# Performance work log

Measured on AMD Instinct MI355X. Metric: run time of the kernel, lower is better.

## Reference

```python
import jax, jax.numpy as jnp
import numpy as np

NUM_CAPSULES = 16
IN_DIM = 512
OUT_DIM = 32
ROUTING_ITERS = 3
EPS = 1e-08


def setup_inputs() -> dict:
    key = jax.random.key(0)
    kx, kw = jax.random.split(key)
    x = jax.random.normal(kx, (32768, IN_DIM), dtype=jnp.float32)
    W = jax.random.normal(kw, (IN_DIM, NUM_CAPSULES * OUT_DIM), dtype=jnp.float32)
    return {"x": x, "W": W}


def squash(s):
    # s: [batch, out_dim]
    norm = jnp.sum(s * s, axis=-1, keepdims=True)
    scale = norm / (1.0 + norm)
    return scale * s / (jnp.sqrt(norm) + EPS)


def reference(x, W):
    batch = x.shape[0]
    # u: [batch, num_capsules, out_dim]
    u = jnp.matmul(x, W).reshape(batch, NUM_CAPSULES, OUT_DIM)
    b = jnp.zeros((batch, NUM_CAPSULES), dtype=x.dtype)
    v = None
    for _ in range(ROUTING_ITERS):
        c = jax.nn.softmax(b, axis=1)[..., None]       # [batch, caps, 1]
        s = jnp.sum(c * u, axis=1)                      # [batch, out_dim]
        v = squash(s)                                   # [batch, out_dim]
        b = b + jnp.sum(u * v[:, None, :], axis=-1)     # [batch, caps]
    return v
```

## Files before the change

### kernel.cpp

```cpp
#include <hip/hip_runtime.h>
#include <math.h>


#define BATCH   32768
#define KDIM    512
#define NDIM    512
#define OUT_DIM 32
#define EPS_F   1e-8f
#define NKT     32

typedef _Float16 half8  __attribute__((ext_vector_type(8)));
typedef _Float16 half4t __attribute__((ext_vector_type(4)));
typedef float   floatx4 __attribute__((ext_vector_type(4)));
typedef float  floatx16 __attribute__((ext_vector_type(16)));

template <int CTRL>
__device__ __forceinline__ float dpp_mov(float x) {
    return __int_as_float(__builtin_amdgcn_mov_dpp(__float_as_int(x), CTRL, 0xF, 0xF, true));
}
template <int XMASK>
__device__ __forceinline__ float swz_xor(float x) {
    return __int_as_float(__builtin_amdgcn_ds_swizzle(__float_as_int(x), (XMASK << 10) | 31));
}
#define ROR4  0x124
#define ROR8  0x128
#define QXOR1 0xB1
#define QXOR2 0x4E

__device__ __forceinline__ float cap_sum(float x) {
    x += dpp_mov<ROR4>(x);
    x += dpp_mov<ROR8>(x);
    x += swz_xor<16>(x);
    x += __shfl_xor(x, 32);
    return x;
}
__device__ __forceinline__ float cap_max(float x) {
    x = fmaxf(x, dpp_mov<ROR4>(x));
    x = fmaxf(x, dpp_mov<ROR8>(x));
    x = fmaxf(x, swz_xor<16>(x));
    x = fmaxf(x, __shfl_xor(x, 32));
    return x;
}
__device__ __forceinline__ float dg_sum(float x) {
    x += dpp_mov<QXOR1>(x);
    x += dpp_mov<QXOR2>(x);
    return x;
}

__global__ void prep_w(const float* __restrict__ W, _Float16* __restrict__ Wh,
                       _Float16* __restrict__ Wl) {
    __shared__ float tile[32][33];
    const int tx = threadIdx.x, ty = threadIdx.y;
    const int n0 = blockIdx.x * 32, k0 = blockIdx.y * 32;
#pragma unroll
    for (int i = 0; i < 4; ++i)
        tile[ty + 8 * i][tx] = W[(size_t)(k0 + ty + 8 * i) * NDIM + n0 + tx];
    __syncthreads();
#pragma unroll
    for (int i = 0; i < 4; ++i) {
        const int k = k0 + tx, n = n0 + ty + 8 * i;
        const float v = tile[tx][ty + 8 * i];
        const _Float16 h = (_Float16)v;
        const _Float16 l = (_Float16)(v - (float)h);
        const size_t off = (size_t)(k >> 4) * (NDIM * 16) + (size_t)n * 16 + (k & 15);
        Wh[off] = h;
        Wl[off] = l;
    }
}

__device__ __forceinline__ void ld_g2l_16(void* lds_base_uniform, const void* g) {
    __builtin_amdgcn_global_load_lds(
        (const __attribute__((address_space(1))) void*)g,
        (__attribute__((address_space(3))) void*)lds_base_uniform, 16, 0, 0);
}

#define AS_OFF 65536

__global__ __launch_bounds__(256, 2)
void capsule_mfma(const float* __restrict__ x, const _Float16* __restrict__ Wh,
                  const _Float16* __restrict__ Wl, float* __restrict__ out) {
    __shared__ __align__(16) char smem[73728];
    _Float16 (*Bs)[2][NDIM][16] = (_Float16 (*)[2][NDIM][16])smem;
    float (*u_lds)[520] = (float (*)[520])smem;

    const int tid  = threadIdx.x;
    const int w    = tid >> 6;
    const int lane = tid & 63;
    const int ln = lane & 31, q = lane >> 5;
    const int rowBlk = blockIdx.x * 64;
    const int C0 = w * 128;

    floatx16 acc[2][4];
#pragma unroll
    for (int mf = 0; mf < 2; ++mf)
#pragma unroll
        for (int nt = 0; nt < 4; ++nt)
#pragma unroll
            for (int i = 0; i < 16; ++i) acc[mf][nt][i] = 0.f;

    const int srow = tid >> 2;
    const int skq  = tid & 3;
    const float* sga = x + (size_t)(rowBlk + srow) * KDIM + skq * 4;
    const int ssw = (srow >> 1) & 3;
    const int swoff_h = srow * 64 + (((skq >> 1) ^ ssw) * 16) + (skq & 1) * 8;
    const int swoff_l = srow * 64 + ((((skq >> 1) ^ 2) ^ ssw) * 16) + (skq & 1) * 8;

    int afr_h[2], afr_l[2];
#pragma unroll
    for (int mf = 0; mf < 2; ++mf) {
        const int ar = mf * 32 + ln;
        const int asw = (ar >> 1) & 3;
        afr_h[mf] = ar * 64 + ((q ^ asw) * 16);
        afr_l[mf] = ar * 64 + (((q ^ 2) ^ asw) * 16);
    }

    const int nseg = w * 128;

    {
        const floatx4 v0 = *(const floatx4*)sga;
        half4t h4, l4;
#pragma unroll
        for (int j = 0; j < 4; ++j) {
            h4[j] = (_Float16)v0[j];
            l4[j] = (_Float16)(v0[j] - (float)h4[j]);
        }
        *(half4t*)(smem + AS_OFF + swoff_h) = h4;
        *(half4t*)(smem + AS_OFF + swoff_l) = l4;
    }
#pragma unroll
    for (int i = 0; i < 4; ++i) {
        ld_g2l_16(&Bs[0][0][nseg + i * 32][0], Wh + (size_t)(nseg + i * 32) * 16 + lane * 8);
        ld_g2l_16(&Bs[0][1][nseg + i * 32][0], Wl + (size_t)(nseg + i * 32) * 16 + lane * 8);
    }

#pragma unroll 2
    for (int kt = 0; kt < NKT; ++kt) {
        __syncthreads();
        const int buf = kt & 1;
        floatx4 sv;
        if (kt + 1 < NKT) {
            sv = *(const floatx4*)(sga + (kt + 1) * 16);
            const size_t g = (size_t)(kt + 1) * (NDIM * 16);
#pragma unroll
            for (int i = 0; i < 4; ++i) {
                ld_g2l_16(&Bs[buf ^ 1][0][nseg + i * 32][0], Wh + g + (size_t)(nseg + i * 32) * 16 + lane * 8);
                ld_g2l_16(&Bs[buf ^ 1][1][nseg + i * 32][0], Wl + g + (size_t)(nseg + i * 32) * 16 + lane * 8);
            }
        }
        const int abase = AS_OFF + buf * 4096;
        half8 ah[2], al[2];
#pragma unroll
        for (int mf = 0; mf < 2; ++mf) {
            ah[mf] = *(const half8*)(smem + abase + afr_h[mf]);
            al[mf] = *(const half8*)(smem + abase + afr_l[mf]);
        }
#pragma unroll
        for (int nt = 0; nt < 4; ++nt) {
            const half8 bh = *(const half8*)&Bs[buf][0][C0 + nt * 32 + ln][q * 8];
            const half8 bl = *(const half8*)&Bs[buf][1][C0 + nt * 32 + ln][q * 8];
#pragma unroll
            for (int mf = 0; mf < 2; ++mf) {
                acc[mf][nt] = __builtin_amdgcn_mfma_f32_32x32x16_f16(ah[mf], bh, acc[mf][nt], 0, 0, 0);
                acc[mf][nt] = __builtin_amdgcn_mfma_f32_32x32x16_f16(al[mf], bh, acc[mf][nt], 0, 0, 0);
                acc[mf][nt] = __builtin_amdgcn_mfma_f32_32x32x16_f16(ah[mf], bl, acc[mf][nt], 0, 0, 0);
            }
        }
        if (kt + 1 < NKT) {
            half4t h4, l4;
#pragma unroll
            for (int j = 0; j < 4; ++j) {
                h4[j] = (_Float16)sv[j];
                l4[j] = (_Float16)(sv[j] - (float)h4[j]);
            }
            const int nbase = AS_OFF + (buf ^ 1) * 4096;
            *(half4t*)(smem + nbase + swoff_h) = h4;
            *(half4t*)(smem + nbase + swoff_l) = l4;
        }
    }

    const int dgrp = lane & 3;
#pragma unroll
    for (int p = 0; p < 2; ++p) {
        __syncthreads();
        {
            const int mf = p;
#pragma unroll
            for (int nt = 0; nt < 4; ++nt)
#pragma unroll
                for (int reg = 0; reg < 16; ++reg)
                    u_lds[(reg & 3) + 8 * (reg >> 2) + 4 * q][C0 + nt * 32 + ln] = acc[mf][nt][reg];
        }
        __syncthreads();
#pragma unroll 1
        for (int ri = 0; ri < 8; ++ri) {
            const int rl = w * 8 + ri;
            const floatx4 ua = *(const floatx4*)&u_lds[rl][lane * 8];
            const floatx4 ub = *(const floatx4*)&u_lds[rl][lane * 8 + 4];
            const float u8[8] = {ua[0], ua[1], ua[2], ua[3],
                                 ub[0], ub[1], ub[2], ub[3]};
            float b_own = 0.f;
            float v[8];
#pragma unroll
            for (int it = 0; it < 3; ++it) {
                float c_own;
                if (it == 0) {
                    c_own = 1.0f / 16.0f;
                } else {
                    const float m = cap_max(b_own);
                    const float e = __expf(b_own - m);
                    const float ssum = cap_sum(e);
                    c_own = e / ssum;
                }
                float s[8];
#pragma unroll
                for (int j = 0; j < 8; ++j) s[j] = c_own * u8[j];
#pragma unroll
                for (int j = 0; j < 8; ++j) s[j] += dpp_mov<ROR4>(s[j]);
#pragma unroll
                for (int j = 0; j < 8; ++j) s[j] += dpp_mov<ROR8>(s[j]);
#pragma unroll
                for (int j = 0; j < 8; ++j) s[j] += swz_xor<16>(s[j]);
#pragma unroll
                for (int j = 0; j < 8; ++j) s[j] += __shfl_xor(s[j], 32);
                float nrm = 0.f;
#pragma unroll
                for (int j = 0; j < 8; ++j) nrm = fmaf(s[j], s[j], nrm);
                nrm = dg_sum(nrm);
                const float scale = nrm / ((1.f + nrm) * (sqrtf(nrm) + EPS_F));
#pragma unroll
                for (int j = 0; j < 8; ++j) v[j] = scale * s[j];
                if (it < 2) {
                    float dot = 0.f;
#pragma unroll
                    for (int j = 0; j < 8; ++j) dot = fmaf(u8[j], v[j], dot);
                    dot = dg_sum(dot);
                    b_own += dot;
                }
            }
            if (lane < 4) {
                float4* o = (float4*)(out + (size_t)(rowBlk + p * 32 + rl) * OUT_DIM
                                      + dgrp * 8);
                o[0] = make_float4(v[0], v[1], v[2], v[3]);
                o[1] = make_float4(v[4], v[5], v[6], v[7]);
            }
        }
    }
}

extern "C" void kernel_launch(void* const* d_in, const int* in_sizes, int n_in,
                              void* d_out, int out_size, void* d_ws, size_t ws_size,
                              hipStream_t stream) {
    const float* x = (const float*)d_in[0];
    const float* W = (const float*)d_in[1];
    float* out = (float*)d_out;
    _Float16* Wh = (_Float16*)d_ws;
    _Float16* Wl = Wh + (size_t)NDIM * KDIM;

    prep_w<<<dim3(16, 16), dim3(32, 8), 0, stream>>>(W, Wh, Wl);
    capsule_mfma<<<dim3(BATCH / 64), dim3(256), 0, stream>>>(x, Wh, Wl, out);
}
```

Measured before the change: 158.3 us.

## Load W fragments directly from global into registers and stage A in 8-kstep superblocks

Drops the LDS staging of the pre-split fp16 W tiles. Each wave now loads its B fragments straight from global memory into registers, double-buffered one fragment ahead of the MFMAs. The x tile is now staged in LDS as 8-k-step superblocks (four of them, double-buffered) with one barrier per superblock instead of one per k-step. The aim is to cut barrier count and LDS traffic for B; the cost is global-load latency sitting on the MFMA critical path, with W reads going through L2 per wave.

Measured after the change: 156.6 us. About the same (-1.1%).

```diff
diff --git a/kernel.cpp b/kernel.cpp
--- a/kernel.cpp
+++ b/kernel.cpp
@@ -8,6 +8,8 @@
 #define OUT_DIM 32
 #define EPS_F   1e-8f
 #define NKT     32
+#define KPS     8
+#define NSB     4
 
 typedef _Float16 half8  __attribute__((ext_vector_type(8)));
 typedef _Float16 half4t __attribute__((ext_vector_type(4)));
@@ -68,19 +70,10 @@
     }
 }
 
-__device__ __forceinline__ void ld_g2l_16(void* lds_base_uniform, const void* g) {
-    __builtin_amdgcn_global_load_lds(
-        (const __attribute__((address_space(1))) void*)g,
-        (__attribute__((address_space(3))) void*)lds_base_uniform, 16, 0, 0);
-}
-
-#define AS_OFF 65536
-
 __global__ __launch_bounds__(256, 2)
 void capsule_mfma(const float* __restrict__ x, const _Float16* __restrict__ Wh,
                   const _Float16* __restrict__ Wl, float* __restrict__ out) {
-    __shared__ __align__(16) char smem[73728];
-    _Float16 (*Bs)[2][NDIM][16] = (_Float16 (*)[2][NDIM][16])smem;
+    __shared__ __align__(16) char smem[66560];
     float (*u_lds)[520] = (float (*)[520])smem;
 
     const int tid  = threadIdx.x;
@@ -98,84 +91,104 @@
 #pragma unroll
             for (int i = 0; i < 16; ++i) acc[mf][nt][i] = 0.f;
 
-    const int srow = tid >> 2;
-    const int skq  = tid & 3;
-    const float* sga = x + (size_t)(rowBlk + srow) * KDIM + skq * 4;
-    const int ssw = (srow >> 1) & 3;
-    const int swoff_h = srow * 64 + (((skq >> 1) ^ ssw) * 16) + (skq & 1) * 8;
-    const int swoff_l = srow * 64 + ((((skq >> 1) ^ 2) ^ ssw) * 16) + (skq & 1) * 8;
-
-    int afr_h[2], afr_l[2];
-#pragma unroll
-    for (int mf = 0; mf < 2; ++mf) {
-        const int ar = mf * 32 + ln;
-        const int asw = (ar >> 1) & 3;
-        afr_h[mf] = ar * 64 + ((q ^ asw) * 16);
-        afr_l[mf] = ar * 64 + (((q ^ 2) ^ asw) * 16);
-    }
-
-    const int nseg = w * 128;
+    const int srow0 = tid >> 5;
+    const int sf    = tid & 31;
+    const int skt   = sf >> 2;
+    const int skq   = sf & 3;
+    const float* aga = x + (size_t)(rowBlk + srow0) * KDIM + skt * 16 + skq * 4;
+    const int ssw = (srow0 >> 1) & 3;
+    const int woffh = skt * 4096 + srow0 * 64 + (((skq >> 1) ^ ssw) * 16) + (skq & 1) * 8;
+
+    const int hoff0 = ln * 64 + ((q ^ ((ln >> 1) & 3)) * 16);
+
+    const int boff = (C0 + ln) * 16 + q * 8;
 
     {
-        const floatx4 v0 = *(const floatx4*)sga;
-        half4t h4, l4;
-#pragma unroll
-        for (int j = 0; j < 4; ++j) {
-            h4[j] = (_Float16)v0[j];
-            l4[j] = (_Float16)(v0[j] - (float)h4[j]);
-        }
-        *(half4t*)(smem + AS_OFF + swoff_h) = h4;
-        *(half4t*)(smem + AS_OFF + swoff_l) = l4;
-    }
-#pragma unroll
-    for (int i = 0; i < 4; ++i) {
-        ld_g2l_16(&Bs[0][0][nseg + i * 32][0], Wh + (size_t)(nseg + i * 32) * 16 + lane * 8);
-        ld_g2l_16(&Bs[0][1][nseg + i * 32][0], Wl + (size_t)(nseg + i * 32) * 16 + lane * 8);
-    }
-
-#pragma unroll 2
-    for (int kt = 0; kt < NKT; ++kt) {
+        floatx4 s0[8];
+#pragma unroll
+        for (int i = 0; i < 8; ++i)
+            s0[i] = *(const floatx4*)(aga + (size_t)(8 * i) * KDIM);
+#pragma unroll
+        for (int i = 0; i < 8; ++i) {
+            half4t h4, l4;
+#pragma unroll
+            for (int j = 0; j < 4; ++j) {
+                h4[j] = (_Float16)s0[i][j];
+                l4[j] = (_Float16)(s0[i][j] - (float)h4[j]);
+            }
+            *(half4t*)(smem + woffh + i * 512)        = h4;
+            *(half4t*)(smem + (woffh ^ 32) + i * 512) = l4;
+        }
+    }
+    half8 bh[2], bl[2];
+    bh[0] = *(const half8*)(Wh + boff);
+    bl[0] = *(const half8*)(Wl + boff);
+
+#define COMPUTE_KK(kk)                                                          \
+    {                                                                           \
+        const int kt = s * KPS + (kk);                                          \
+        const char* ab = smem + abuf + (kk) * 4096;                             \
+        const half8 ah0 = *(const half8*)(ab + hoff0);                          \
+        const half8 al0 = *(const half8*)(ab + (hoff0 ^ 32));                   \
+        const half8 ah1 = *(const half8*)(ab + hoff0 + 2048);                   \
+        const half8 al1 = *(const half8*)(ab + ((hoff0 + 2048) ^ 32));          \
+        _Pragma("unroll")                                                       \
+        for (int nt = 0; nt < 4; ++nt) {                                        \
+            const int cu = nt & 1, nx = cu ^ 1;                                 \
+            const int kn = (nt < 3) ? kt : ((kt + 1 < NKT) ? kt + 1 : kt);      \
+            const int nn = (nt < 3) ? nt + 1 : 0;                               \
+            bh[nx] = *(const half8*)(Wh + (size_t)kn * 8192 + nn * 512 + boff); \
+            bl[nx] = *(const half8*)(Wl + (size_t)kn * 8192 + nn * 512 + boff); \
+            acc[0][nt] = __builtin_amdgcn_mfma_f32_32x32x16_f16(ah0, bh[cu], acc[0][nt], 0, 0, 0); \
+            acc[0][nt] = __builtin_amdgcn_mfma_f32_32x32x16_f16(al0, bh[cu], acc[0][nt], 0, 0, 0); \
+            acc[0][nt] = __builtin_amdgcn_mfma_f32_32x32x16_f16(ah0, bl[cu], acc[0][nt], 0, 0, 0); \
+            acc[1][nt] = __builtin_amdgcn_mfma_f32_32x32x16_f16(ah1, bh[cu], acc[1][nt], 0, 0, 0); \
+            acc[1][nt] = __builtin_amdgcn_mfma_f32_32x32x16_f16(al1, bh[cu], acc[1][nt], 0, 0, 0); \
+            acc[1][nt] = __builtin_amdgcn_mfma_f32_32x32x16_f16(ah1, bl[cu], acc[1][nt], 0, 0, 0); \
+        }                                                                       \
+    }
+
+#define STAGE_HALF(h0)                                                          \
+    {                                                                           \
+        half4t h4, l4;                                                          \
+        _Pragma("unroll")                                                       \
+        for (int i = 0; i < 4; ++i) {                                           \
+            _Pragma("unroll")                                                   \
+            for (int j = 0; j < 4; ++j) {                                       \
+                h4[j] = (_Float16)sv[i][j];                                     \
+                l4[j] = (_Float16)(sv[i][j] - (float)h4[j]);                    \
+            }                                                                   \
+            *(half4t*)(smem + nbuf + woffh + ((h0) + i) * 512)        = h4;     \
+            *(half4t*)(smem + nbuf + ((woffh ^ 32)) + ((h0) + i) * 512) = l4;   \
+        }                                                                       \
+    }
+
+#pragma unroll 1
+    for (int s = 0; s < NSB; ++s) {
         __syncthreads();
-        const int buf = kt & 1;
-        floatx4 sv;
-        if (kt + 1 < NKT) {
-            sv = *(const floatx4*)(sga + (kt + 1) * 16);
-            const size_t g = (size_t)(kt + 1) * (NDIM * 16);
-#pragma unroll
-            for (int i = 0; i < 4; ++i) {
-                ld_g2l_16(&Bs[buf ^ 1][0][nseg + i * 32][0], Wh + g + (size_t)(nseg + i * 32) * 16 + lane * 8);
-                ld_g2l_16(&Bs[buf ^ 1][1][nseg + i * 32][0], Wl + g + (size_t)(nseg + i * 32) * 16 + lane * 8);
-            }
-        }
-        const int abase = AS_OFF + buf * 4096;
-        half8 ah[2], al[2];
-#pragma unroll
-        for (int mf = 0; mf < 2; ++mf) {
-            ah[mf] = *(const half8*)(smem + abase + afr_h[mf]);
-            al[mf] = *(const half8*)(smem + abase + afr_l[mf]);
-        }
-#pragma unroll
-        for (int nt = 0; nt < 4; ++nt) {
-            const half8 bh = *(const half8*)&Bs[buf][0][C0 + nt * 32 + ln][q * 8];
-            const half8 bl = *(const half8*)&Bs[buf][1][C0 + nt * 32 + ln][q * 8];
-#pragma unroll
-            for (int mf = 0; mf < 2; ++mf) {
-                acc[mf][nt] = __builtin_amdgcn_mfma_f32_32x32x16_f16(ah[mf], bh, acc[mf][nt], 0, 0, 0);
-                acc[mf][nt] = __builtin_amdgcn_mfma_f32_32x32x16_f16(al[mf], bh, acc[mf][nt], 0, 0, 0);
-                acc[mf][nt] = __builtin_amdgcn_mfma_f32_32x32x16_f16(ah[mf], bl, acc[mf][nt], 0, 0, 0);
-            }
-        }
-        if (kt + 1 < NKT) {
-            half4t h4, l4;
-#pragma unroll
-            for (int j = 0; j < 4; ++j) {
-                h4[j] = (_Float16)sv[j];
-                l4[j] = (_Float16)(sv[j] - (float)h4[j]);
-            }
-            const int nbase = AS_OFF + (buf ^ 1) * 4096;
-            *(half4t*)(smem + nbase + swoff_h) = h4;
-            *(half4t*)(smem + nbase + swoff_l) = l4;
-        }
+        const int abuf = (s & 1) * 32768;
+        const int nbuf = abuf ^ 32768;
+        floatx4 sv[4];
+        if (s + 1 < NSB) {
+#pragma unroll
+            for (int i = 0; i < 4; ++i)
+                sv[i] = *(const floatx4*)(aga + (size_t)(s + 1) * 128 + (size_t)(8 * i) * KDIM);
+        }
+        COMPUTE_KK(0)
+        COMPUTE_KK(1)
+        if (s + 1 < NSB) STAGE_HALF(0)
+        if (s + 1 < NSB) {
+#pragma unroll
+            for (int i = 0; i < 4; ++i)
+                sv[i] = *(const floatx4*)(aga + (size_t)(s + 1) * 128 + (size_t)(8 * (i + 4)) * KDIM);
+        }
+        COMPUTE_KK(2)
+        COMPUTE_KK(3)
+        COMPUTE_KK(4)
+        COMPUTE_KK(5)
+        if (s + 1 < NSB) STAGE_HALF(4)
+        COMPUTE_KK(6)
+        COMPUTE_KK(7)
     }
 
     const int dgrp = lane & 3;
@@ -211,24 +224,24 @@
                     const float ssum = cap_sum(e);
                     c_own = e / ssum;
                 }
-                float s[8];
-#pragma unroll
-                for (int j = 0; j < 8; ++j) s[j] = c_own * u8[j];
-#pragma unroll
-                for (int j = 0; j < 8; ++j) s[j] += dpp_mov<ROR4>(s[j]);
-#pragma unroll
-                for (int j = 0; j < 8; ++j) s[j] += dpp_mov<ROR8>(s[j]);
-#pragma unroll
-                for (int j = 0; j < 8; ++j) s[j] += swz_xor<16>(s[j]);
-#pragma unroll
-                for (int j = 0; j < 8; ++j) s[j] += __shfl_xor(s[j], 32);
+                float s8[8];
+#pragma unroll
+                for (int j = 0; j < 8; ++j) s8[j] = c_own * u8[j];
+#pragma unroll
+                for (int j = 0; j < 8; ++j) s8[j] += dpp_mov<ROR4>(s8[j]);
+#pragma unroll
+                for (int j = 0; j < 8; ++j) s8[j] += dpp_mov<ROR8>(s8[j]);
+#pragma unroll
+                for (int j = 0; j < 8; ++j) s8[j] += swz_xor<16>(s8[j]);
+#pragma unroll
+                for (int j = 0; j < 8; ++j) s8[j] += __shfl_xor(s8[j], 32);
                 float nrm = 0.f;
 #pragma unroll
-                for (int j = 0; j < 8; ++j) nrm = fmaf(s[j], s[j], nrm);
+                for (int j = 0; j < 8; ++j) nrm = fmaf(s8[j], s8[j], nrm);
                 nrm = dg_sum(nrm);
                 const float scale = nrm / ((1.f + nrm) * (sqrtf(nrm) + EPS_F));
 #pragma unroll
-                for (int j = 0; j < 8; ++j) v[j] = scale * s[j];
+                for (int j = 0; j < 8; ++j) v[j] = scale * s8[j];
                 if (it < 2) {
                     float dot = 0.f;
 #pragma unroll
```
